# Performance work log

Hardware: AMD Instinct MI355X
Metric: run time of the kernel (lower is better)

The kernel has to match this reference:

```python
import jax, jax.numpy as jnp
import numpy as np

B, N, D, H = 8, 2048, 32, 4
HD = D // H  # head_dim = 8
LN_EPS = 1e-5


def setup_inputs() -> dict:
    key = jax.random.key(0)
    ks = jax.random.split(key, 6)
    x = jax.random.normal(ks[0], (B, N, D), dtype=jnp.float32)
    adj_raw = jax.random.uniform(ks[1], (N, N), dtype=jnp.float32)
    adj_prior = adj_raw / (adj_raw.sum(axis=-1, keepdims=True) + 1e-8)
    Wqkv = jax.random.normal(ks[2], (D, 3 * D), dtype=jnp.float32) * (1.0 / np.sqrt(D))
    bqkv = jnp.zeros((3 * D,), dtype=jnp.float32)
    Wout = jax.random.normal(ks[3], (D, D), dtype=jnp.float32) * (1.0 / np.sqrt(D))
    bout = jnp.zeros((D,), dtype=jnp.float32)
    gamma = jnp.ones((D,), dtype=jnp.float32)
    beta = jnp.zeros((D,), dtype=jnp.float32)
    geo_weight = jnp.float32(0.3)
    return {"x": x, "adj_prior": adj_prior, "geo_weight": geo_weight,
            "Wqkv": Wqkv, "bqkv": bqkv, "Wout": Wout, "bout": bout,
            "gamma": gamma, "beta": beta}


def reference(x, adj_prior, geo_weight, Wqkv, bqkv, Wout, bout, gamma, beta):
    b, n, d = x.shape
    qkv = x @ Wqkv + bqkv                        # [B,N,3D]
    qkv = qkv.reshape(b, n, 3, H, HD)
    qkv = jnp.transpose(qkv, (2, 0, 3, 1, 4))    # [3,B,H,N,HD]
    q, k, v = qkv[0], qkv[1], qkv[2]
    scores = jnp.einsum('bhnd,bhmd->bhnm', q, k) / jnp.sqrt(jnp.float32(HD))
    blend = jax.nn.sigmoid(geo_weight)
    scores = (1.0 - blend) * scores + blend * adj_prior[None, None] * 5.0
    w = jax.nn.softmax(scores, axis=-1)          # dropout omitted (eval mode)
    out = jnp.einsum('bhnm,bhmd->bhnd', w, v)    # [B,H,N,HD]
    out = jnp.transpose(out, (0, 2, 1, 3)).reshape(b, n, d)
    out = out @ Wout + bout
    res = out + x
    mu = res.mean(axis=-1, keepdims=True)
    var = res.var(axis=-1, keepdims=True)
    return (res - mu) * jax.lax.rsqrt(var + LN_EPS) * gamma + beta
```

## Files before the change

kernel.cpp:

```cpp
#include <hip/hip_runtime.h>


typedef _Float16 f16;
typedef _Float16 f16x4 __attribute__((ext_vector_type(4)));
typedef _Float16 f16x8 __attribute__((ext_vector_type(8)));
typedef __fp16 h16x2 __attribute__((ext_vector_type(2)));
typedef __fp16 h16x8 __attribute__((ext_vector_type(8)));
typedef float f32x4 __attribute__((ext_vector_type(4)));

__global__ __launch_bounds__(256) void prep_qkv_kernel(
    const float* __restrict__ x, const float* __restrict__ Wqkv,
    const float* __restrict__ bqkv, const float* __restrict__ adj,
    const float* __restrict__ gw_p, f16* __restrict__ q16,
    f16* __restrict__ kf_ws, f16* __restrict__ vf_ws,
    f16* __restrict__ adj16) {
  const float LOG2E = 1.4426950408889634f;
  float blend = 1.f / (1.f + __expf(-gw_p[0]));
  int tid = threadIdx.x;
  __shared__ float Ws[32 * 96];
  __shared__ float bsh[96];
  __shared__ float xs[16 * 32];

  if (blockIdx.x < 2048) {
    float c2 = blend * 5.f * LOG2E;
    int gid = blockIdx.x * 256 + tid;
    int tile = gid >> 6, lane = gid & 63;
    int qtp = tile >> 7, jt = tile & 127;
    int col = jt * 16 + (lane >> 4) * 4;
    f32x4 v0 = *(const f32x4*)(adj + (size_t)(qtp * 32 + (lane & 15)) * 2048 + col);
    f32x4 v1 = *(const f32x4*)(adj + (size_t)(qtp * 32 + 16 + (lane & 15)) * 2048 + col);
    f16x8 r;
    r[0] = (f16)__builtin_amdgcn_exp2f(c2 * v0[0]);
    r[1] = (f16)__builtin_amdgcn_exp2f(c2 * v0[1]);
    r[2] = (f16)__builtin_amdgcn_exp2f(c2 * v0[2]);
    r[3] = (f16)__builtin_amdgcn_exp2f(c2 * v0[3]);
    r[4] = (f16)__builtin_amdgcn_exp2f(c2 * v1[0]);
    r[5] = (f16)__builtin_amdgcn_exp2f(c2 * v1[1]);
    r[6] = (f16)__builtin_amdgcn_exp2f(c2 * v1[2]);
    r[7] = (f16)__builtin_amdgcn_exp2f(c2 * v1[3]);
    *(f16x8*)(adj16 + (size_t)gid * 8) = r;
    if (gid < 262144) {
      const f16x4 z = {};
      if (lane >= 32) *(f16x4*)(kf_ws + (size_t)gid * 4) = z;
      int dq = lane & 15;
      if (dq == 8) {
        f16x4 ones = {(f16)1.f, (f16)1.f, (f16)1.f, (f16)1.f};
        *(f16x4*)(vf_ws + (size_t)gid * 4) = ones;
      } else if (dq > 8) {
        *(f16x4*)(vf_ws + (size_t)gid * 4) = z;
      }
    }
  } else {
    float c1 = (1.f - blend) * 0.35355339059327373f * LOG2E;
    int blk = blockIdx.x - 2048;
    for (int i = tid; i < 32 * 96; i += 256) Ws[i] = Wqkv[i];
    if (tid < 96) bsh[tid] = bqkv[tid];
    int rowbase = blk * 16;
    for (int i = tid; i < 16 * 32; i += 256) xs[i] = x[rowbase * 32 + i];
    __syncthreads();
#pragma unroll
    for (int e = 0; e < 6; ++e) {
      int idx = tid + e * 256;
      int r = idx / 96, c = idx % 96;
      float acc = bsh[c];
#pragma unroll
      for (int k = 0; k < 32; ++k) acc += xs[r * 32 + k] * Ws[k * 96 + c];
      int nrow = rowbase + r;
      int b = nrow >> 11, n = nrow & 2047;
      int s = c >> 5, h = (c >> 3) & 3, d = c & 7;
      int bh = b * 4 + h;
      int jt = n >> 4, jr = n & 15;
      if (s == 0) {
        q16[((size_t)bh * 2048 + n) * 8 + d] = (f16)(acc * c1);
      } else if (s == 1) {
        int lane = ((d >> 2) << 4) | jr;
        kf_ws[(((size_t)bh * 128 + jt) * 64 + lane) * 4 + (d & 3)] = (f16)acc;
      } else {
        int lane = ((jr >> 2) << 4) | d;
        vf_ws[(((size_t)bh * 128 + jt) * 64 + lane) * 4 + (jr & 3)] = (f16)acc;
      }
    }
  }
}

__global__ __launch_bounds__(512, 4) void attn_kernel(
    const f16* __restrict__ q16, const f16* __restrict__ kf_ws,
    const f16* __restrict__ vf_ws, const f16* __restrict__ adj16,
    float* __restrict__ attn_ws) {
  int blk = blockIdx.x;
  int chunk = blk & 7;
  int within = blk >> 3;
  int bhp = within & 15;
  int qtq = (chunk << 2) | (within >> 4);
  int tid = threadIdx.x;
  int w = tid >> 6, lane = tid & 63;
  int lq = lane & 15, lh = lane >> 4;
  int bh0 = bhp * 2;
  int jt0 = w * 16;

  const f16* kp0 = kf_ws + (((size_t)bh0 * 128 + jt0) * 64 + lane) * 4;
  const f16* kp1 = kp0 + (size_t)128 * 64 * 4;
  const f16* vp0 = vf_ws + (((size_t)bh0 * 128 + jt0) * 64 + lane) * 4;
  const f16* vp1 = vp0 + (size_t)128 * 64 * 4;
  const f16* ap0 = adj16 + (((size_t)(qtq * 2) * 128 + jt0) * 64 + lane) * 8;
  const f16* ap1 = ap0 + (size_t)128 * 64 * 8;

  f16x4 qf[2][4];
#pragma unroll
  for (int u = 0; u < 2; ++u)
#pragma unroll
    for (int m = 0; m < 4; ++m) {
      f16x4 t = {};
      if (lane < 32)
        t = *(const f16x4*)(q16 + ((size_t)(bh0 + u) * 2048 +
                                   (qtq * 4 + m) * 16 + lq) * 8 + lh * 4);
      qf[u][m] = t;
    }

  f32x4 acc[2][4];
#pragma unroll
  for (int u = 0; u < 2; ++u)
#pragma unroll
    for (int m = 0; m < 4; ++m) acc[u][m] = (f32x4){0.f, 0.f, 0.f, 0.f};
  const f32x4 zero4 = {0.f, 0.f, 0.f, 0.f};

#pragma unroll 4
  for (int t = 0; t < 16; ++t) {
    f16x4 kf0 = *(const f16x4*)(kp0 + t * 256);
    f16x4 kf1 = *(const f16x4*)(kp1 + t * 256);
    f16x4 vf0 = *(const f16x4*)(vp0 + t * 256);
    f16x4 vf1 = *(const f16x4*)(vp1 + t * 256);
    h16x8 av0 = *(const h16x8*)(ap0 + t * 512);
    h16x8 av1 = *(const h16x8*)(ap1 + t * 512);
#pragma unroll
    for (int u = 0; u < 2; ++u) {
      f16x4 kfu = u ? kf1 : kf0;
      f16x4 vfu = u ? vf1 : vf0;
#pragma unroll
      for (int m = 0; m < 4; ++m) {
        f32x4 s = __builtin_amdgcn_mfma_f32_16x16x16f16(kfu, qf[u][m], zero4, 0, 0, 0);
        h16x8 av = (m < 2) ? av0 : av1;
        int b4 = (m & 1) * 4;
        float e0 = __builtin_amdgcn_exp2f(s[0]);
        float e1 = __builtin_amdgcn_exp2f(s[1]);
        float e2 = __builtin_amdgcn_exp2f(s[2]);
        float e3 = __builtin_amdgcn_exp2f(s[3]);
        h16x2 p01 = __builtin_amdgcn_cvt_pkrtz(e0, e1);
        h16x2 p23 = __builtin_amdgcn_cvt_pkrtz(e2, e3);
        h16x2 ea01 = {av[b4 + 0], av[b4 + 1]};
        h16x2 ea23 = {av[b4 + 2], av[b4 + 3]};
        p01 *= ea01;
        p23 *= ea23;
        f16x4 pa;
        pa[0] = (f16)(float)p01[0]; pa[1] = (f16)(float)p01[1];
        pa[2] = (f16)(float)p23[0]; pa[3] = (f16)(float)p23[1];
        acc[u][m] = __builtin_amdgcn_mfma_f32_16x16x16f16(pa, vfu, acc[u][m], 0, 0, 0);
      }
    }
  }

  __shared__ f32x4 mlds[8][8][64];
#pragma unroll
  for (int u = 0; u < 2; ++u)
#pragma unroll
    for (int m = 0; m < 4; ++m) mlds[w][u * 4 + m][lane] = acc[u][m];
  __syncthreads();
  int p = w;
  f32x4 sum = mlds[0][p][lane];
#pragma unroll
  for (int s = 1; s < 8; ++s) {
    f32x4 o = mlds[s][p][lane];
    sum[0] += o[0]; sum[1] += o[1]; sum[2] += o[2]; sum[3] += o[3];
  }
  int dsrc = (lane & 48) | 8;
  float d0 = __shfl(sum[0], dsrc);
  float d1 = __shfl(sum[1], dsrc);
  float d2 = __shfl(sum[2], dsrc);
  float d3 = __shfl(sum[3], dsrc);
  if (lq < 8) {
    int bh = bh0 + (p >> 2);
    int b = bh >> 2, h = bh & 3;
    int qt0 = (qtq * 4 + (p & 3)) * 16;
    size_t base = ((size_t)b * 2048 + qt0 + lh * 4) * 32 + h * 8 + lq;
    attn_ws[base]      = sum[0] / d0;
    attn_ws[base + 32] = sum[1] / d1;
    attn_ws[base + 64] = sum[2] / d2;
    attn_ws[base + 96] = sum[3] / d3;
  }
}

__global__ __launch_bounds__(256) void out_ln_kernel(
    const float* __restrict__ attn_ws, const float* __restrict__ x,
    const float* __restrict__ Wout, const float* __restrict__ bout,
    const float* __restrict__ gamma, const float* __restrict__ beta,
    float* __restrict__ out) {
  __shared__ float Ws[32 * 32];
  __shared__ float bs[32], gs[32], bts[32];
  int tid = threadIdx.x;
  for (int i = tid; i < 1024; i += 256) Ws[i] = Wout[i];
  if (tid < 32) { bs[tid] = bout[tid]; gs[tid] = gamma[tid]; bts[tid] = beta[tid]; }
  __syncthreads();
  int row = blockIdx.x * 8 + (tid >> 5);
  int d = tid & 31;
  const float* ar = attn_ws + (size_t)row * 32;
  float acc = bs[d];
#pragma unroll
  for (int k = 0; k < 32; ++k) acc += ar[k] * Ws[k * 32 + d];
  float res = acc + x[(size_t)row * 32 + d];
  float s1 = res, s2 = res * res;
#pragma unroll
  for (int off = 16; off >= 1; off >>= 1) {
    s1 += __shfl_xor(s1, off);
    s2 += __shfl_xor(s2, off);
  }
  float mu = s1 * 0.03125f;
  float var = s2 * 0.03125f - mu * mu;
  float r = rsqrtf(var + 1e-5f);
  out[(size_t)row * 32 + d] = (res - mu) * r * gs[d] + bts[d];
}

extern "C" void kernel_launch(void* const* d_in, const int* in_sizes, int n_in,
                              void* d_out, int out_size, void* d_ws, size_t ws_size,
                              hipStream_t stream) {
  const float* x     = (const float*)d_in[0];
  const float* adj   = (const float*)d_in[1];
  const float* gw    = (const float*)d_in[2];
  const float* Wqkv  = (const float*)d_in[3];
  const float* bqkv  = (const float*)d_in[4];
  const float* Wout  = (const float*)d_in[5];
  const float* bout  = (const float*)d_in[6];
  const float* gamma = (const float*)d_in[7];
  const float* beta  = (const float*)d_in[8];
  float* out = (float*)d_out;

  char* wsb = (char*)d_ws;
  f16* q16       = (f16*)wsb;
  f16* kf_ws     = (f16*)(wsb + (1 << 20));
  f16* vf_ws     = (f16*)(wsb + (3 << 20));
  f16* adj16     = (f16*)(wsb + (5 << 20));
  float* attn_ws = (float*)(wsb + (13 << 20));

  prep_qkv_kernel<<<3072, 256, 0, stream>>>(x, Wqkv, bqkv, adj, gw,
                                            q16, kf_ws, vf_ws, adj16);
  attn_kernel<<<512, 512, 0, stream>>>(q16, kf_ws, vf_ws, adj16, attn_ws);
  out_ln_kernel<<<2048, 256, 0, stream>>>(attn_ws, x, Wout, bout, gamma, beta, out);
}
```

Measured before the change: 47.08 us.

## Split attention key range across blocks and reduce partial sums in output kernel

Each attention block now covers 4 batch-heads and 2 query tiles over half of the key range, where before it covered 2 batch-heads and 4 query tiles over all keys. Each block loads one adjacency fragment per step and shares it across 4 heads, cutting adjacency traffic, which is the largest input stream. The two key halves write separate numerator and denominator partials to workspace. The output/LayerNorm kernel adds the partials and divides before the projection. This costs more workspace writes and reads and a smaller intra-block reduction.

Result: slower. 54.81 us (+16.4%).

```diff
diff --git a/kernel.cpp b/kernel.cpp
--- a/kernel.cpp
+++ b/kernel.cpp
@@ -86,61 +86,61 @@
 __global__ __launch_bounds__(512, 4) void attn_kernel(
     const f16* __restrict__ q16, const f16* __restrict__ kf_ws,
     const f16* __restrict__ vf_ws, const f16* __restrict__ adj16,
-    float* __restrict__ attn_ws) {
+    float* __restrict__ num_ws, float* __restrict__ den_ws) {
   int blk = blockIdx.x;
   int chunk = blk & 7;
   int within = blk >> 3;
-  int bhp = within & 15;
-  int qtq = (chunk << 2) | (within >> 4);
+  int qtg = chunk * 4 + (within >> 4);
+  int bhjt = within & 15;
+  int bhg = bhjt & 7;
+  int jth = bhjt >> 3;
   int tid = threadIdx.x;
   int w = tid >> 6, lane = tid & 63;
+  int qth = w & 1, jq = w >> 1;
   int lq = lane & 15, lh = lane >> 4;
-  int bh0 = bhp * 2;
-  int jt0 = w * 16;
-
-  const f16* kp0 = kf_ws + (((size_t)bh0 * 128 + jt0) * 64 + lane) * 4;
-  const f16* kp1 = kp0 + (size_t)128 * 64 * 4;
-  const f16* vp0 = vf_ws + (((size_t)bh0 * 128 + jt0) * 64 + lane) * 4;
-  const f16* vp1 = vp0 + (size_t)128 * 64 * 4;
-  const f16* ap0 = adj16 + (((size_t)(qtq * 2) * 128 + jt0) * 64 + lane) * 8;
-  const f16* ap1 = ap0 + (size_t)128 * 64 * 8;
-
-  f16x4 qf[2][4];
-#pragma unroll
-  for (int u = 0; u < 2; ++u)
-#pragma unroll
-    for (int m = 0; m < 4; ++m) {
+  int bh0 = bhg * 4;
+  int jt0 = jth * 64 + jq * 16;
+  int qtp = qtg * 2 + qth;
+  int qt0 = qtp * 2;
+
+  const f16* kp = kf_ws + (((size_t)bh0 * 128 + jt0) * 64 + lane) * 4;
+  const f16* vp = vf_ws + (((size_t)bh0 * 128 + jt0) * 64 + lane) * 4;
+  const f16* ap = adj16 + (((size_t)qtp * 128 + jt0) * 64 + lane) * 8;
+
+  f16x4 qf[4][2];
+#pragma unroll
+  for (int u = 0; u < 4; ++u)
+#pragma unroll
+    for (int m = 0; m < 2; ++m) {
       f16x4 t = {};
       if (lane < 32)
         t = *(const f16x4*)(q16 + ((size_t)(bh0 + u) * 2048 +
-                                   (qtq * 4 + m) * 16 + lq) * 8 + lh * 4);
+                                   (qt0 + m) * 16 + lq) * 8 + lh * 4);
       qf[u][m] = t;
     }
 
-  f32x4 acc[2][4];
-#pragma unroll
-  for (int u = 0; u < 2; ++u)
-#pragma unroll
-    for (int m = 0; m < 4; ++m) acc[u][m] = (f32x4){0.f, 0.f, 0.f, 0.f};
+  f32x4 acc[4][2];
+#pragma unroll
+  for (int u = 0; u < 4; ++u)
+#pragma unroll
+    for (int m = 0; m < 2; ++m) acc[u][m] = (f32x4){0.f, 0.f, 0.f, 0.f};
   const f32x4 zero4 = {0.f, 0.f, 0.f, 0.f};
 
-#pragma unroll 4
+#pragma unroll 2
   for (int t = 0; t < 16; ++t) {
-    f16x4 kf0 = *(const f16x4*)(kp0 + t * 256);
-    f16x4 kf1 = *(const f16x4*)(kp1 + t * 256);
-    f16x4 vf0 = *(const f16x4*)(vp0 + t * 256);
-    f16x4 vf1 = *(const f16x4*)(vp1 + t * 256);
-    h16x8 av0 = *(const h16x8*)(ap0 + t * 512);
-    h16x8 av1 = *(const h16x8*)(ap1 + t * 512);
-#pragma unroll
-    for (int u = 0; u < 2; ++u) {
-      f16x4 kfu = u ? kf1 : kf0;
-      f16x4 vfu = u ? vf1 : vf0;
-#pragma unroll
-      for (int m = 0; m < 4; ++m) {
-        f32x4 s = __builtin_amdgcn_mfma_f32_16x16x16f16(kfu, qf[u][m], zero4, 0, 0, 0);
-        h16x8 av = (m < 2) ? av0 : av1;
-        int b4 = (m & 1) * 4;
+    f16x4 kf[4], vf[4];
+#pragma unroll
+    for (int u = 0; u < 4; ++u) {
+      kf[u] = *(const f16x4*)(kp + u * 32768 + t * 256);
+      vf[u] = *(const f16x4*)(vp + u * 32768 + t * 256);
+    }
+    h16x8 av = *(const h16x8*)(ap + t * 512);
+#pragma unroll
+    for (int u = 0; u < 4; ++u) {
+#pragma unroll
+      for (int m = 0; m < 2; ++m) {
+        f32x4 s = __builtin_amdgcn_mfma_f32_16x16x16f16(kf[u], qf[u][m], zero4, 0, 0, 0);
+        int b4 = m * 4;
         float e0 = __builtin_amdgcn_exp2f(s[0]);
         float e1 = __builtin_amdgcn_exp2f(s[1]);
         float e2 = __builtin_amdgcn_exp2f(s[2]);
@@ -154,55 +154,78 @@
         f16x4 pa;
         pa[0] = (f16)(float)p01[0]; pa[1] = (f16)(float)p01[1];
         pa[2] = (f16)(float)p23[0]; pa[3] = (f16)(float)p23[1];
-        acc[u][m] = __builtin_amdgcn_mfma_f32_16x16x16f16(pa, vfu, acc[u][m], 0, 0, 0);
-      }
-    }
-  }
-
-  __shared__ f32x4 mlds[8][8][64];
-#pragma unroll
-  for (int u = 0; u < 2; ++u)
-#pragma unroll
-    for (int m = 0; m < 4; ++m) mlds[w][u * 4 + m][lane] = acc[u][m];
+        acc[u][m] = __builtin_amdgcn_mfma_f32_16x16x16f16(pa, vf[u], acc[u][m], 0, 0, 0);
+      }
+    }
+  }
+
+  __shared__ f32x4 mlds[2][3][8][64];
+  if (jq) {
+#pragma unroll
+    for (int u = 0; u < 4; ++u)
+#pragma unroll
+      for (int m = 0; m < 2; ++m) mlds[qth][jq - 1][u * 2 + m][lane] = acc[u][m];
+  }
   __syncthreads();
-  int p = w;
-  f32x4 sum = mlds[0][p][lane];
-#pragma unroll
-  for (int s = 1; s < 8; ++s) {
-    f32x4 o = mlds[s][p][lane];
-    sum[0] += o[0]; sum[1] += o[1]; sum[2] += o[2]; sum[3] += o[3];
-  }
-  int dsrc = (lane & 48) | 8;
-  float d0 = __shfl(sum[0], dsrc);
-  float d1 = __shfl(sum[1], dsrc);
-  float d2 = __shfl(sum[2], dsrc);
-  float d3 = __shfl(sum[3], dsrc);
-  if (lq < 8) {
-    int bh = bh0 + (p >> 2);
-    int b = bh >> 2, h = bh & 3;
-    int qt0 = (qtq * 4 + (p & 3)) * 16;
-    size_t base = ((size_t)b * 2048 + qt0 + lh * 4) * 32 + h * 8 + lq;
-    attn_ws[base]      = sum[0] / d0;
-    attn_ws[base + 32] = sum[1] / d1;
-    attn_ws[base + 64] = sum[2] / d2;
-    attn_ws[base + 96] = sum[3] / d3;
+  if (jq == 0) {
+#pragma unroll
+    for (int p = 0; p < 3; ++p)
+#pragma unroll
+      for (int u = 0; u < 4; ++u)
+#pragma unroll
+        for (int m = 0; m < 2; ++m) {
+          f32x4 o = mlds[qth][p][u * 2 + m][lane];
+          acc[u][m][0] += o[0]; acc[u][m][1] += o[1];
+          acc[u][m][2] += o[2]; acc[u][m][3] += o[3];
+        }
+    size_t joff = (size_t)jth << 19;
+#pragma unroll
+    for (int u = 0; u < 4; ++u) {
+#pragma unroll
+      for (int m = 0; m < 2; ++m) {
+        f32x4 s = acc[u][m];
+        int qt = qt0 + m;
+        int n0 = qt * 16 + lh * 4;
+        if (lq < 8) {
+          size_t base = joff + ((size_t)bhg * 2048 + n0) * 32 + u * 8 + lq;
+          num_ws[base]      = s[0];
+          num_ws[base + 32] = s[1];
+          num_ws[base + 64] = s[2];
+          num_ws[base + 96] = s[3];
+        } else if (lq == 8) {
+          size_t dbase = ((size_t)jth << 16) + ((size_t)(bh0 + u)) * 2048 + n0;
+          den_ws[dbase]     = s[0];
+          den_ws[dbase + 1] = s[1];
+          den_ws[dbase + 2] = s[2];
+          den_ws[dbase + 3] = s[3];
+        }
+      }
+    }
   }
 }
 
 __global__ __launch_bounds__(256) void out_ln_kernel(
-    const float* __restrict__ attn_ws, const float* __restrict__ x,
-    const float* __restrict__ Wout, const float* __restrict__ bout,
-    const float* __restrict__ gamma, const float* __restrict__ beta,
-    float* __restrict__ out) {
+    const float* __restrict__ num_ws, const float* __restrict__ den_ws,
+    const float* __restrict__ x, const float* __restrict__ Wout,
+    const float* __restrict__ bout, const float* __restrict__ gamma,
+    const float* __restrict__ beta, float* __restrict__ out) {
   __shared__ float Ws[32 * 32];
   __shared__ float bs[32], gs[32], bts[32];
+  __shared__ float arow[8][32];
   int tid = threadIdx.x;
   for (int i = tid; i < 1024; i += 256) Ws[i] = Wout[i];
   if (tid < 32) { bs[tid] = bout[tid]; gs[tid] = gamma[tid]; bts[tid] = beta[tid]; }
-  __syncthreads();
   int row = blockIdx.x * 8 + (tid >> 5);
   int d = tid & 31;
-  const float* ar = attn_ws + (size_t)row * 32;
+  int b = row >> 11, n = row & 2047;
+  int h = d >> 3;
+  float num = num_ws[(size_t)row * 32 + d] +
+              num_ws[(1u << 19) + (size_t)row * 32 + d];
+  float den = den_ws[((size_t)(b * 4 + h)) * 2048 + n] +
+              den_ws[(1u << 16) + ((size_t)(b * 4 + h)) * 2048 + n];
+  arow[tid >> 5][d] = num / den;
+  __syncthreads();
+  const float* ar = arow[tid >> 5];
   float acc = bs[d];
 #pragma unroll
   for (int k = 0; k < 32; ++k) acc += ar[k] * Ws[k * 32 + d];
@@ -238,10 +261,12 @@
   f16* kf_ws     = (f16*)(wsb + (1 << 20));
   f16* vf_ws     = (f16*)(wsb + (3 << 20));
   f16* adj16     = (f16*)(wsb + (5 << 20));
-  float* attn_ws = (float*)(wsb + (13 << 20));
+  float* num_ws  = (float*)(wsb + (13 << 20));
+  float* den_ws  = (float*)(wsb + (17 << 20));
 
   prep_qkv_kernel<<<3072, 256, 0, stream>>>(x, Wqkv, bqkv, adj, gw,
                                             q16, kf_ws, vf_ws, adj16);
-  attn_kernel<<<512, 512, 0, stream>>>(q16, kf_ws, vf_ws, adj16, attn_ws);
-  out_ln_kernel<<<2048, 256, 0, stream>>>(attn_ws, x, Wout, bout, gamma, beta, out);
-}
+  attn_kernel<<<512, 512, 0, stream>>>(q16, kf_ws, vf_ws, adj16, num_ws, den_ws);
+  out_ln_kernel<<<2048, 256, 0, stream>>>(num_ws, den_ws, x, Wout, bout,
+                                          gamma, beta, out);
+}
```

## Stage adj tiles through LDS and pair K/V tiles into 16-byte fragments

Applied to the files above, without the earlier changes.

The adjacency prep now reads whole 32x256 row chunks from adj with coalesced float4 loads into shared memory, then builds the swizzled fp16 exp tiles from LDS. It uses 512 blocks that each process four outputs per thread, where before 2048 blocks did strided global reads. The K/V workspace layout interleaves two consecutive 16-key tiles so the attention kernel can issue one 16-byte load instead of two 8-byte loads. The loop is restructured to 8 iterations handling two tiles each. This adds an LDS round trip and a barrier in the prep kernel, and raises register pressure in the attention loop.

Result: no change. 46.22 us (-1.8%).

```diff
diff --git a/kernel.cpp b/kernel.cpp
--- a/kernel.cpp
+++ b/kernel.cpp
@@ -17,54 +17,65 @@
   const float LOG2E = 1.4426950408889634f;
   float blend = 1.f / (1.f + __expf(-gw_p[0]));
   int tid = threadIdx.x;
-  __shared__ float Ws[32 * 96];
-  __shared__ float bsh[96];
-  __shared__ float xs[16 * 32];
-
-  if (blockIdx.x < 2048) {
+  __shared__ union {
+    float als[32][260];
+    struct { float Ws[32 * 96]; float bsh[96]; float xs[16 * 32]; } qk;
+  } u;
+
+  if (blockIdx.x < 512) {
+    int g = blockIdx.x * 256 + tid;
+    int glane = g & 63;
+    const f16x8 z8 = {};
+    if (glane >= 32) *(f16x8*)(kf_ws + (size_t)g * 8) = z8;
+    int glq = glane & 15;
+    if (glq == 8) {
+      f16x8 o8 = {(f16)1.f, (f16)1.f, (f16)1.f, (f16)1.f,
+                  (f16)1.f, (f16)1.f, (f16)1.f, (f16)1.f};
+      *(f16x8*)(vf_ws + (size_t)g * 8) = o8;
+    } else if (glq > 8) {
+      *(f16x8*)(vf_ws + (size_t)g * 8) = z8;
+    }
     float c2 = blend * 5.f * LOG2E;
-    int gid = blockIdx.x * 256 + tid;
-    int tile = gid >> 6, lane = gid & 63;
-    int qtp = tile >> 7, jt = tile & 127;
-    int col = jt * 16 + (lane >> 4) * 4;
-    f32x4 v0 = *(const f32x4*)(adj + (size_t)(qtp * 32 + (lane & 15)) * 2048 + col);
-    f32x4 v1 = *(const f32x4*)(adj + (size_t)(qtp * 32 + 16 + (lane & 15)) * 2048 + col);
-    f16x8 r;
-    r[0] = (f16)__builtin_amdgcn_exp2f(c2 * v0[0]);
-    r[1] = (f16)__builtin_amdgcn_exp2f(c2 * v0[1]);
-    r[2] = (f16)__builtin_amdgcn_exp2f(c2 * v0[2]);
-    r[3] = (f16)__builtin_amdgcn_exp2f(c2 * v0[3]);
-    r[4] = (f16)__builtin_amdgcn_exp2f(c2 * v1[0]);
-    r[5] = (f16)__builtin_amdgcn_exp2f(c2 * v1[1]);
-    r[6] = (f16)__builtin_amdgcn_exp2f(c2 * v1[2]);
-    r[7] = (f16)__builtin_amdgcn_exp2f(c2 * v1[3]);
-    *(f16x8*)(adj16 + (size_t)gid * 8) = r;
-    if (gid < 262144) {
-      const f16x4 z = {};
-      if (lane >= 32) *(f16x4*)(kf_ws + (size_t)gid * 4) = z;
-      int dq = lane & 15;
-      if (dq == 8) {
-        f16x4 ones = {(f16)1.f, (f16)1.f, (f16)1.f, (f16)1.f};
-        *(f16x4*)(vf_ws + (size_t)gid * 4) = ones;
-      } else if (dq > 8) {
-        *(f16x4*)(vf_ws + (size_t)gid * 4) = z;
-      }
+    int qtp = blockIdx.x >> 3;
+    int chunk = blockIdx.x & 7;
+    const float* src = adj + (size_t)(qtp * 32) * 2048 + chunk * 256;
+#pragma unroll
+    for (int i = 0; i < 8; ++i) {
+      int idx = i * 1024 + tid * 4;
+      int row = idx >> 8, col = idx & 255;
+      f32x4 v = *(const f32x4*)(src + (size_t)row * 2048 + col);
+      *(f32x4*)&u.als[row][col] = v;
+    }
+    __syncthreads();
+#pragma unroll
+    for (int i = 0; i < 4; ++i) {
+      int flat = i * 256 + tid;
+      int jt_l = flat >> 6, lane = flat & 63;
+      int lq = lane & 15, lh = lane >> 4;
+      int col0 = jt_l * 16 + lh * 4;
+      f16x8 r;
+#pragma unroll
+      for (int e = 0; e < 8; ++e)
+        r[e] = (f16)__builtin_amdgcn_exp2f(
+            c2 * u.als[(e < 4 ? 0 : 16) + lq][col0 + (e & 3)]);
+      int jt = chunk * 16 + jt_l;
+      *(f16x8*)(adj16 + (((size_t)qtp * 128 + jt) * 64 + lane) * 8) = r;
     }
   } else {
     float c1 = (1.f - blend) * 0.35355339059327373f * LOG2E;
-    int blk = blockIdx.x - 2048;
-    for (int i = tid; i < 32 * 96; i += 256) Ws[i] = Wqkv[i];
-    if (tid < 96) bsh[tid] = bqkv[tid];
+    int blk = blockIdx.x - 512;
+    for (int i = tid; i < 32 * 96; i += 256) u.qk.Ws[i] = Wqkv[i];
+    if (tid < 96) u.qk.bsh[tid] = bqkv[tid];
     int rowbase = blk * 16;
-    for (int i = tid; i < 16 * 32; i += 256) xs[i] = x[rowbase * 32 + i];
+    for (int i = tid; i < 16 * 32; i += 256) u.qk.xs[i] = x[rowbase * 32 + i];
     __syncthreads();
 #pragma unroll
     for (int e = 0; e < 6; ++e) {
       int idx = tid + e * 256;
       int r = idx / 96, c = idx % 96;
-      float acc = bsh[c];
-#pragma unroll
-      for (int k = 0; k < 32; ++k) acc += xs[r * 32 + k] * Ws[k * 96 + c];
+      float acc = u.qk.bsh[c];
+#pragma unroll
+      for (int k = 0; k < 32; ++k) acc += u.qk.xs[r * 32 + k] * u.qk.Ws[k * 96 + c];
       int nrow = rowbase + r;
       int b = nrow >> 11, n = nrow & 2047;
       int s = c >> 5, h = (c >> 3) & 3, d = c & 7;
@@ -74,10 +85,12 @@
         q16[((size_t)bh * 2048 + n) * 8 + d] = (f16)(acc * c1);
       } else if (s == 1) {
         int lane = ((d >> 2) << 4) | jr;
-        kf_ws[(((size_t)bh * 128 + jt) * 64 + lane) * 4 + (d & 3)] = (f16)acc;
+        kf_ws[(((size_t)bh * 64 + (jt >> 1)) * 64 + lane) * 8 +
+              (jt & 1) * 4 + (d & 3)] = (f16)acc;
       } else {
         int lane = ((jr >> 2) << 4) | d;
-        vf_ws[(((size_t)bh * 128 + jt) * 64 + lane) * 4 + (jr & 3)] = (f16)acc;
+        vf_ws[(((size_t)bh * 64 + (jt >> 1)) * 64 + lane) * 8 +
+              (jt & 1) * 4 + (jr & 3)] = (f16)acc;
       }
     }
   }
@@ -96,74 +109,82 @@
   int w = tid >> 6, lane = tid & 63;
   int lq = lane & 15, lh = lane >> 4;
   int bh0 = bhp * 2;
-  int jt0 = w * 16;
-
-  const f16* kp0 = kf_ws + (((size_t)bh0 * 128 + jt0) * 64 + lane) * 4;
-  const f16* kp1 = kp0 + (size_t)128 * 64 * 4;
-  const f16* vp0 = vf_ws + (((size_t)bh0 * 128 + jt0) * 64 + lane) * 4;
-  const f16* vp1 = vp0 + (size_t)128 * 64 * 4;
-  const f16* ap0 = adj16 + (((size_t)(qtq * 2) * 128 + jt0) * 64 + lane) * 8;
+
+  const f16* kp = kf_ws + (((size_t)bh0 * 64 + w * 8) * 64 + lane) * 8;
+  const f16* vp = vf_ws + (((size_t)bh0 * 64 + w * 8) * 64 + lane) * 8;
+  const f16* ap0 = adj16 + (((size_t)(qtq * 2) * 128 + w * 16) * 64 + lane) * 8;
   const f16* ap1 = ap0 + (size_t)128 * 64 * 8;
 
   f16x4 qf[2][4];
 #pragma unroll
-  for (int u = 0; u < 2; ++u)
+  for (int uu = 0; uu < 2; ++uu)
 #pragma unroll
     for (int m = 0; m < 4; ++m) {
       f16x4 t = {};
       if (lane < 32)
-        t = *(const f16x4*)(q16 + ((size_t)(bh0 + u) * 2048 +
+        t = *(const f16x4*)(q16 + ((size_t)(bh0 + uu) * 2048 +
                                    (qtq * 4 + m) * 16 + lq) * 8 + lh * 4);
-      qf[u][m] = t;
+      qf[uu][m] = t;
     }
 
   f32x4 acc[2][4];
 #pragma unroll
-  for (int u = 0; u < 2; ++u)
-#pragma unroll
-    for (int m = 0; m < 4; ++m) acc[u][m] = (f32x4){0.f, 0.f, 0.f, 0.f};
+  for (int uu = 0; uu < 2; ++uu)
+#pragma unroll
+    for (int m = 0; m < 4; ++m) acc[uu][m] = (f32x4){0.f, 0.f, 0.f, 0.f};
   const f32x4 zero4 = {0.f, 0.f, 0.f, 0.f};
 
-#pragma unroll 4
-  for (int t = 0; t < 16; ++t) {
-    f16x4 kf0 = *(const f16x4*)(kp0 + t * 256);
-    f16x4 kf1 = *(const f16x4*)(kp1 + t * 256);
-    f16x4 vf0 = *(const f16x4*)(vp0 + t * 256);
-    f16x4 vf1 = *(const f16x4*)(vp1 + t * 256);
-    h16x8 av0 = *(const h16x8*)(ap0 + t * 512);
-    h16x8 av1 = *(const h16x8*)(ap1 + t * 512);
-#pragma unroll
-    for (int u = 0; u < 2; ++u) {
-      f16x4 kfu = u ? kf1 : kf0;
-      f16x4 vfu = u ? vf1 : vf0;
-#pragma unroll
-      for (int m = 0; m < 4; ++m) {
-        f32x4 s = __builtin_amdgcn_mfma_f32_16x16x16f16(kfu, qf[u][m], zero4, 0, 0, 0);
-        h16x8 av = (m < 2) ? av0 : av1;
-        int b4 = (m & 1) * 4;
-        float e0 = __builtin_amdgcn_exp2f(s[0]);
-        float e1 = __builtin_amdgcn_exp2f(s[1]);
-        float e2 = __builtin_amdgcn_exp2f(s[2]);
-        float e3 = __builtin_amdgcn_exp2f(s[3]);
-        h16x2 p01 = __builtin_amdgcn_cvt_pkrtz(e0, e1);
-        h16x2 p23 = __builtin_amdgcn_cvt_pkrtz(e2, e3);
-        h16x2 ea01 = {av[b4 + 0], av[b4 + 1]};
-        h16x2 ea23 = {av[b4 + 2], av[b4 + 3]};
-        p01 *= ea01;
-        p23 *= ea23;
-        f16x4 pa;
-        pa[0] = (f16)(float)p01[0]; pa[1] = (f16)(float)p01[1];
-        pa[2] = (f16)(float)p23[0]; pa[3] = (f16)(float)p23[1];
-        acc[u][m] = __builtin_amdgcn_mfma_f32_16x16x16f16(pa, vfu, acc[u][m], 0, 0, 0);
+#pragma unroll 2
+  for (int tp = 0; tp < 8; ++tp) {
+    f16x8 kf80 = *(const f16x8*)(kp + tp * 512);
+    f16x8 kf81 = *(const f16x8*)(kp + 32768 + tp * 512);
+    f16x8 vf80 = *(const f16x8*)(vp + tp * 512);
+    f16x8 vf81 = *(const f16x8*)(vp + 32768 + tp * 512);
+    h16x8 a0a = *(const h16x8*)(ap0 + (tp * 2) * 512);
+    h16x8 a0b = *(const h16x8*)(ap0 + (tp * 2 + 1) * 512);
+    h16x8 a1a = *(const h16x8*)(ap1 + (tp * 2) * 512);
+    h16x8 a1b = *(const h16x8*)(ap1 + (tp * 2 + 1) * 512);
+#pragma unroll
+    for (int jh = 0; jh < 2; ++jh) {
+      f16x4 kf0 = {kf80[jh * 4], kf80[jh * 4 + 1], kf80[jh * 4 + 2], kf80[jh * 4 + 3]};
+      f16x4 kf1 = {kf81[jh * 4], kf81[jh * 4 + 1], kf81[jh * 4 + 2], kf81[jh * 4 + 3]};
+      f16x4 vf0 = {vf80[jh * 4], vf80[jh * 4 + 1], vf80[jh * 4 + 2], vf80[jh * 4 + 3]};
+      f16x4 vf1 = {vf81[jh * 4], vf81[jh * 4 + 1], vf81[jh * 4 + 2], vf81[jh * 4 + 3]};
+      h16x8 av0 = jh ? a0b : a0a;
+      h16x8 av1 = jh ? a1b : a1a;
+#pragma unroll
+      for (int uu = 0; uu < 2; ++uu) {
+        f16x4 kfu = uu ? kf1 : kf0;
+        f16x4 vfu = uu ? vf1 : vf0;
+#pragma unroll
+        for (int m = 0; m < 4; ++m) {
+          f32x4 s = __builtin_amdgcn_mfma_f32_16x16x16f16(kfu, qf[uu][m], zero4, 0, 0, 0);
+          h16x8 av = (m < 2) ? av0 : av1;
+          int b4 = (m & 1) * 4;
+          float e0 = __builtin_amdgcn_exp2f(s[0]);
+          float e1 = __builtin_amdgcn_exp2f(s[1]);
+          float e2 = __builtin_amdgcn_exp2f(s[2]);
+          float e3 = __builtin_amdgcn_exp2f(s[3]);
+          h16x2 p01 = __builtin_amdgcn_cvt_pkrtz(e0, e1);
+          h16x2 p23 = __builtin_amdgcn_cvt_pkrtz(e2, e3);
+          h16x2 ea01 = {av[b4 + 0], av[b4 + 1]};
+          h16x2 ea23 = {av[b4 + 2], av[b4 + 3]};
+          p01 *= ea01;
+          p23 *= ea23;
+          f16x4 pa;
+          pa[0] = (f16)(float)p01[0]; pa[1] = (f16)(float)p01[1];
+          pa[2] = (f16)(float)p23[0]; pa[3] = (f16)(float)p23[1];
+          acc[uu][m] = __builtin_amdgcn_mfma_f32_16x16x16f16(pa, vfu, acc[uu][m], 0, 0, 0);
+        }
       }
     }
   }
 
   __shared__ f32x4 mlds[8][8][64];
 #pragma unroll
-  for (int u = 0; u < 2; ++u)
-#pragma unroll
-    for (int m = 0; m < 4; ++m) mlds[w][u * 4 + m][lane] = acc[u][m];
+  for (int uu = 0; uu < 2; ++uu)
+#pragma unroll
+    for (int m = 0; m < 4; ++m) mlds[w][uu * 4 + m][lane] = acc[uu][m];
   __syncthreads();
   int p = w;
   f32x4 sum = mlds[0][p][lane];
@@ -240,7 +261,7 @@
   f16* adj16     = (f16*)(wsb + (5 << 20));
   float* attn_ws = (float*)(wsb + (13 << 20));
 
-  prep_qkv_kernel<<<3072, 256, 0, stream>>>(x, Wqkv, bqkv, adj, gw,
+  prep_qkv_kernel<<<1536, 256, 0, stream>>>(x, Wqkv, bqkv, adj, gw,
                                             q16, kf_ws, vf_ws, adj16);
   attn_kernel<<<512, 512, 0, stream>>>(q16, kf_ws, vf_ws, adj16, attn_ws);
   out_ln_kernel<<<2048, 256, 0, stream>>>(attn_ws, x, Wout, bout, gamma, beta, out);
```
